# Kernel optimization log

Hardware: AMD Instinct MI355X
Metric: run time of the kernel (lower is better)

Reference implementation:

```python
import jax, jax.numpy as jnp
import numpy as np

N, E, F, H, L, G, C, NC = 100000, 1200000, 32, 64, 3, 256, 200000, 10
D = L * H  # concat node embedding dim = 192


def setup_inputs() -> dict:
    key = jax.random.key(0)
    ks = jax.random.split(key, 20)

    def w(k, shape):
        fan_in = shape[-2] if len(shape) > 1 else shape[0]
        return jax.random.normal(k, shape, jnp.float32) * (1.0 / np.sqrt(fan_in))

    inp = dict(
        x=jax.random.normal(ks[0], (N, F), jnp.float32),
        edge_index=jax.random.randint(ks[1], (2, E), 0, N),
        batch=jnp.sort(jax.random.randint(ks[2], (N,), 0, G)),
        cand_node=jax.random.randint(ks[3], (C,), 0, N),
        c1_W1=w(ks[4], (F, H)), c1_b1=jnp.zeros((H,)),
        c1_W2=w(ks[5], (H, H)), c1_b2=jnp.zeros((H,)),
        c1_g=jnp.ones((H,)), c1_be=jnp.zeros((H,)), c1_m=jnp.zeros((H,)), c1_v=jnp.ones((H,)),
        c1_eps=jnp.zeros((1,)),
        cs_W1=w(ks[6], (L - 1, H, H)), cs_b1=jnp.zeros((L - 1, H)),
        cs_W2=w(ks[7], (L - 1, H, H)), cs_b2=jnp.zeros((L - 1, H)),
        cs_g=jnp.ones((L - 1, H)), cs_be=jnp.zeros((L - 1, H)),
        cs_m=jnp.zeros((L - 1, H)), cs_v=jnp.ones((L - 1, H)),
        cs_eps=jnp.zeros((L - 1,)),
        nc_W1=w(ks[8], (D, 2 * H)), nc_b1=jnp.zeros((2 * H,)),
        nc_W2=w(ks[9], (2 * H, H)), nc_b2=jnp.zeros((H,)),
        nc_W3=w(ks[10], (H, H)), nc_b3=jnp.zeros((H,)),
        nc_W4=w(ks[11], (H, NC)), nc_b4=jnp.zeros((NC,)),
        comp_emb=jax.random.normal(ks[12], (NC, D), jnp.float32),
        ep_W1=w(ks[13], (2 * D, 2 * H)), ep_b1=jnp.zeros((2 * H,)),
        ep_W2=w(ks[14], (2 * H, H)), ep_b2=jnp.zeros((H,)),
        ep_W3=w(ks[15], (H, 1)), ep_b3=jnp.zeros((1,)),
    )
    return inp


def _bn(h, g, b, m, v):
    # BatchNorm1d in eval mode with running stats
    return g * (h - m) * jax.lax.rsqrt(v + 1e-5) + b


def _gin_layer(h, src, dst, eps, W1, b1, W2, b2, g, be, m, v):
    agg = jax.ops.segment_sum(h[src], dst, num_segments=N)  # sum aggregation
    h = (1.0 + eps) * h + agg
    h = jax.nn.relu(h @ W1 + b1)
    h = jax.nn.relu(h @ W2 + b2)
    return _bn(h, g, be, m, v)


def reference(x, edge_index, batch, cand_node,
              c1_W1, c1_b1, c1_W2, c1_b2, c1_g, c1_be, c1_m, c1_v, c1_eps,
              cs_W1, cs_b1, cs_W2, cs_b2, cs_g, cs_be, cs_m, cs_v, cs_eps,
              nc_W1, nc_b1, nc_W2, nc_b2, nc_W3, nc_b3, nc_W4, nc_b4,
              comp_emb, ep_W1, ep_b1, ep_W2, ep_b2, ep_W3, ep_b3):
    src, dst = edge_index[0], edge_index[1]
    # shared GIN encoder: concat per-layer node embeddings -> [N, L*H]
    h = _gin_layer(x, src, dst, c1_eps, c1_W1, c1_b1, c1_W2, c1_b2, c1_g, c1_be, c1_m, c1_v)
    xs = [h]
    for i in range(cs_W1.shape[0]):
        h = _gin_layer(h, src, dst, cs_eps[i], cs_W1[i], cs_b1[i], cs_W2[i], cs_b2[i],
                       cs_g[i], cs_be[i], cs_m[i], cs_v[i])
        xs.append(h)
    node_emb = jnp.concatenate(xs, axis=-1)  # [N, D]

    # global mean pool per graph -> classification head (dropout=identity in eval)
    sums = jax.ops.segment_sum(node_emb, batch, num_segments=G)
    cnt = jax.ops.segment_sum(jnp.ones((node_emb.shape[0], 1), node_emb.dtype), batch, num_segments=G)
    graph_emb = sums / jnp.maximum(cnt, 1.0)  # [G, D]
    hc = jax.nn.relu(graph_emb @ nc_W1 + nc_b1)
    hc = jax.nn.relu(hc @ nc_W2 + nc_b2)
    hc = jax.nn.relu(hc @ nc_W3 + nc_b3)
    logits = hc @ nc_W4 + nc_b4
    class_output = jax.nn.log_softmax(logits, axis=-1)  # [G, NC]

    # link prediction: predicted comp type per graph, score all candidates in one batch
    comp_idx = jnp.argmax(class_output, axis=-1)          # [G]
    cand_graph = batch[cand_node]                          # [C]
    ce = comp_emb[comp_idx[cand_graph]]                    # [C, D]
    de = node_emb[cand_node]                               # [C, D]
    ef = jnp.concatenate([ce, de], axis=-1)                # [C, 2D]
    he = jax.nn.relu(ef @ ep_W1 + ep_b1)
    he = jax.nn.relu(he @ ep_W2 + ep_b2)
    edge_scores = jax.nn.sigmoid((he @ ep_W3 + ep_b3).squeeze(-1))  # [C]
    return class_output, edge_scores
```

## Files before the change

kernel.cpp:

```cpp
#include <hip/hip_runtime.h>
#include <hip/hip_bf16.h>


#define GG 256
#define NCC 10
#define DD 192
#define BSH 8

typedef short bf16x8 __attribute__((ext_vector_type(8)));
typedef float f32x4  __attribute__((ext_vector_type(4)));

__device__ inline unsigned short f2bf_u(float x) {
    __hip_bfloat16 h = __float2bfloat16(x);
    return *reinterpret_cast<unsigned short*>(&h);
}
__device__ inline float bf2f(unsigned short u) {
    return __uint_as_float(((unsigned int)u) << 16);
}

__global__ void bin_hist(const int* __restrict__ dst, int* __restrict__ bcnt, int E_) {
    __shared__ int h[512];
    const int t = threadIdx.x;
    h[t] = 0; h[t + 256] = 0;
    __syncthreads();
    for (int e = blockIdx.x * 256 + t; e < E_; e += gridDim.x * 256)
        atomicAdd(&h[dst[e] >> BSH], 1);
    __syncthreads();
    if (h[t]) atomicAdd(&bcnt[t], h[t]);
    if (h[t + 256]) atomicAdd(&bcnt[t + 256], h[t + 256]);
}

__global__ void bin_scan(const int* __restrict__ bcnt, int* __restrict__ bbase,
                         int* __restrict__ bpos, int NB, int E_) {
    __shared__ int ps[256];
    const int t = threadIdx.x;
    int v0 = (2 * t < NB) ? bcnt[2 * t] : 0;
    int v1 = (2 * t + 1 < NB) ? bcnt[2 * t + 1] : 0;
    int pv = v0 + v1;
    ps[t] = pv;
    __syncthreads();
    for (int off = 1; off < 256; off <<= 1) {
        int x = (t >= off) ? ps[t - off] : 0;
        __syncthreads();
        ps[t] += x;
        __syncthreads();
    }
    const int excl = ps[t] - pv;
    if (2 * t < NB)     { bbase[2 * t] = excl;          bpos[2 * t] = excl; }
    if (2 * t + 1 < NB) { bbase[2 * t + 1] = excl + v0; bpos[2 * t + 1] = excl + v0; }
    if (t == 0) bbase[NB] = E_;
}

__global__ __launch_bounds__(256) void bin_scatter(
    const int* __restrict__ src, const int* __restrict__ dst,
    int* __restrict__ bpos, unsigned* __restrict__ ebuf, int E_) {
    __shared__ int h[512];
    __shared__ int base[512];
    const int t = threadIdx.x;
    const int e0 = blockIdx.x * 4096;
    h[t] = 0; h[t + 256] = 0;
    __syncthreads();
    int myb[16], myr[16];
    unsigned pk[16];
    #pragma unroll
    for (int u = 0; u < 16; ++u) {
        int e = e0 + t + u * 256;
        if (e < E_) {
            int d = dst[e];
            myb[u] = d >> BSH;
            pk[u] = ((unsigned)src[e] << BSH) | (unsigned)(d & ((1 << BSH) - 1));
            myr[u] = atomicAdd(&h[myb[u]], 1);
        } else myb[u] = -1;
    }
    __syncthreads();
    if (h[t]) base[t] = atomicAdd(&bpos[t], h[t]);
    if (h[t + 256]) base[t + 256] = atomicAdd(&bpos[t + 256], h[t + 256]);
    __syncthreads();
    #pragma unroll
    for (int u = 0; u < 16; ++u)
        if (myb[u] >= 0)
            ebuf[base[myb[u]] + myr[u]] = pk[u];
}

__global__ __launch_bounds__(256) void csr_bucket(
    const unsigned* __restrict__ ebuf, const int* __restrict__ bbase,
    int* __restrict__ rowptr, int* __restrict__ nbr, int N_, int NB) {
    __shared__ int lh[256];
    __shared__ int lx[256];
    __shared__ int ps[256];
    const int b = blockIdx.x;
    const int t = threadIdx.x;
    const int ebase = bbase[b], eend = bbase[b + 1];
    const int ecnt = eend - ebase;
    const int n0 = b << BSH;

    lh[t] = 0;
    __syncthreads();
    for (int i = t; i < ecnt; i += 256)
        atomicAdd(&lh[ebuf[ebase + i] & ((1 << BSH) - 1)], 1);
    __syncthreads();

    int v = lh[t];
    ps[t] = v;
    __syncthreads();
    for (int off = 1; off < 256; off <<= 1) {
        int x = (t >= off) ? ps[t - off] : 0;
        __syncthreads();
        ps[t] += x;
        __syncthreads();
    }
    lx[t] = ps[t] - v;
    {
        int n = n0 + t;
        if (n < N_) rowptr[n] = ebase + lx[t];
    }
    if (b == NB - 1 && t == 0) rowptr[N_] = eend;
    __syncthreads();
    lh[t] = lx[t];
    __syncthreads();
    for (int i = t; i < ecnt; i += 256) {
        unsigned p = ebuf[ebase + i];
        int r = atomicAdd(&lh[p & ((1 << BSH) - 1)], 1);
        nbr[ebase + r] = (int)(p >> BSH);
    }
}

__global__ void x2b_kernel(const float* __restrict__ x, unsigned short* __restrict__ xb,
                           int n_elem) {
    int i = blockIdx.x * 256 + threadIdx.x;
    int stride = gridDim.x * 256;
    for (; i * 4 < n_elem; i += stride) {
        float4 v = *(const float4*)(x + i * 4);
        ushort4 u;
        u.x = f2bf_u(v.x); u.y = f2bf_u(v.y); u.z = f2bf_u(v.z); u.w = f2bf_u(v.w);
        *(ushort4*)(xb + i * 4) = u;
    }
}

__global__ void prep_enc(const float* __restrict__ c1W1, const float* __restrict__ c1W2,
                         const float* __restrict__ csW1, const float* __restrict__ csW2,
                         unsigned short* __restrict__ enc) {
    int idx = blockIdx.x * 256 + threadIdx.x;
    if (idx >= 22528) return;
    const float* W; int rel;
    if (idx < 2048)       { W = c1W1;        rel = idx; }
    else if (idx < 6144)  { W = c1W2;        rel = idx - 2048; }
    else if (idx < 10240) { W = csW1;        rel = idx - 6144; }
    else if (idx < 14336) { W = csW2;        rel = idx - 10240; }
    else if (idx < 18432) { W = csW1 + 4096; rel = idx - 14336; }
    else                  { W = csW2 + 4096; rel = idx - 18432; }
    int frag = rel >> 9;
    int lane = (rel >> 3) & 63;
    int j = rel & 7;
    int ks = frag >> 2, nt = frag & 3;
    int k = ks * 32 + ((lane >> 4) << 3) + j;
    int n = nt * 16 + (lane & 15);
    enc[idx] = f2bf_u(W[k * 64 + n]);
}

__global__ void gcnt_bs(const int* __restrict__ batch, int* __restrict__ gcnt_i, int N_) {
    __shared__ int lbs[GG + 1];
    const int g = threadIdx.x;
    int lo = 0, hi = N_;
    while (lo < hi) {
        int mid = (lo + hi) >> 1;
        if (batch[mid] < g) lo = mid + 1; else hi = mid;
    }
    lbs[g] = lo;
    if (g == 0) lbs[GG] = N_;
    __syncthreads();
    gcnt_i[g] = lbs[g + 1] - lbs[g];
}

#define SWZ(row, byte) ((byte) ^ (((row) & 7) << 4))

#define GSTEP(VCUR, VNXT)                                                     \
    _Pragma("unroll")                                                         \
    for (int u = 0; u < 16; ++u)                                              \
        VNXT[u] = bf2f(*(const unsigned short*)(hbase + (unsigned)idx[u] * (unsigned)RSB + lane2)); \
    _Pragma("unroll")                                                         \
    for (int u = 0; u < 16; ++u) idx[u] = nbp[k + 32 + u];                    \
    {                                                                         \
        float runk = run;                                                     \
        _Pragma("unroll")                                                     \
        for (int u = 0; u < 16; ++u) run += VCUR[u];                          \
        if ((unsigned)(e1 - k) < 16u) { float tt = runk;                      \
            _Pragma("unroll")                                                 \
            for (int u = 0; u < 16; ++u) tt += (u < e1 - k) ? VCUR[u] : 0.f;  \
            s0 = tt; }                                                        \
        if ((unsigned)(e2 - k) < 16u) { float tt = runk;                      \
            _Pragma("unroll")                                                 \
            for (int u = 0; u < 16; ++u) tt += (u < e2 - k) ? VCUR[u] : 0.f;  \
            s1 = tt; }                                                        \
        if ((unsigned)(e3 - k) < 16u) { float tt = runk;                      \
            _Pragma("unroll")                                                 \
            for (int u = 0; u < 16; ++u) tt += (u < e3 - k) ? VCUR[u] : 0.f;  \
            s2 = tt; }                                                        \
        if ((unsigned)(cnt - k) < 16u) { float tt = runk;                     \
            _Pragma("unroll")                                                 \
            for (int u = 0; u < 16; ++u) tt += (u < cnt - k) ? VCUR[u] : 0.f; \
            s3 = tt; }                                                        \
    }                                                                         \
    k += 16;                                                                  \
    if (k > cnt) break;

template<int K>
__global__ __launch_bounds__(512) void gin_fused(
    const unsigned short* __restrict__ hin_b,
    const int* __restrict__ rowptr, const int* __restrict__ nbr,
    const unsigned short* __restrict__ W1p, const float* __restrict__ b1,
    const unsigned short* __restrict__ W2p, const float* __restrict__ b2,
    const float* __restrict__ gamma, const float* __restrict__ beta,
    const float* __restrict__ mean, const float* __restrict__ var,
    const float* __restrict__ eps_p,
    __hip_bfloat16* __restrict__ out_b,
    const int* __restrict__ batch, float* __restrict__ gsum, int soff,
    int N_) {
    __shared__ char s_agg[32 * 128];
    __shared__ char s_h1[32 * 128];
    __shared__ char s_out[32 * 128];
    __shared__ int sb[32];

    const int t = threadIdx.x;
    const int lane = t & 63;
    const int w = t >> 6;
    const int node0 = blockIdx.x * 32;
    const int nb = w * 4;

    if (t < 32) sb[t] = (node0 + t < N_) ? batch[node0 + t] : -1;

    const float eps1 = 1.0f + eps_p[0];

    const int n0w = node0 + nb;
    const int rp0 = __builtin_amdgcn_readfirstlane(rowptr[min(n0w + 0, N_)]);
    const int rp1 = __builtin_amdgcn_readfirstlane(rowptr[min(n0w + 1, N_)]);
    const int rp2 = __builtin_amdgcn_readfirstlane(rowptr[min(n0w + 2, N_)]);
    const int rp3 = __builtin_amdgcn_readfirstlane(rowptr[min(n0w + 3, N_)]);
    const int rp4 = __builtin_amdgcn_readfirstlane(rowptr[min(n0w + 4, N_)]);
    const int cnt = rp4 - rp0;
    const int e1 = rp1 - rp0, e2 = rp2 - rp0, e3 = rp3 - rp0;
    const int* nbp = nbr + rp0;

    const int RSB = (K == 64) ? DD * 2 : 64;
    const int OST = (K == 64) ? DD : 32;
    const char* hbase = (const char*)hin_b;
    const unsigned lane2 = (unsigned)(lane & (K - 1)) * 2u;

    int idx[16];
    float vA[16], vB[16];
    float run = 0.f, s0 = 0.f, s1 = 0.f, s2 = 0.f, s3 = 0.f;
    #pragma unroll
    for (int u = 0; u < 16; ++u) idx[u] = nbp[u];
    #pragma unroll
    for (int u = 0; u < 16; ++u)
        vA[u] = bf2f(*(const unsigned short*)(hbase + (unsigned)idx[u] * (unsigned)RSB + lane2));
    #pragma unroll
    for (int u = 0; u < 16; ++u) idx[u] = nbp[16 + u];
    for (int k = 0;;) {
        GSTEP(vA, vB)
        GSTEP(vB, vA)
    }
    float a0 = s0, a1 = s1 - s0, a2 = s2 - s1, a3 = s3 - s2;
    {
        const unsigned short* hbp = hin_b + (lane & (K - 1));
        if (n0w + 0 < N_) a0 += eps1 * bf2f(hbp[(size_t)(n0w + 0) * OST]);
        if (n0w + 1 < N_) a1 += eps1 * bf2f(hbp[(size_t)(n0w + 1) * OST]);
        if (n0w + 2 < N_) a2 += eps1 * bf2f(hbp[(size_t)(n0w + 2) * OST]);
        if (n0w + 3 < N_) a3 += eps1 * bf2f(hbp[(size_t)(n0w + 3) * OST]);
    }
    if (K == 64 || lane < 32) {
        const int kd = lane & (K - 1);
        *(unsigned short*)(s_agg + SWZ(nb + 0, (nb + 0) * 128 + kd * 2)) = f2bf_u(a0);
        *(unsigned short*)(s_agg + SWZ(nb + 1, (nb + 1) * 128 + kd * 2)) = f2bf_u(a1);
        *(unsigned short*)(s_agg + SWZ(nb + 2, (nb + 2) * 128 + kd * 2)) = f2bf_u(a2);
        *(unsigned short*)(s_agg + SWZ(nb + 3, (nb + 3) * 128 + kd * 2)) = f2bf_u(a3);
    }
    __syncthreads();

    const int mt = w >> 2, nt = w & 3;
    const int arow = mt * 16 + (lane & 15);
    const int col = nt * 16 + (lane & 15);
    f32x4 c1v = (f32x4){0.f, 0.f, 0.f, 0.f};
    #pragma unroll
    for (int ks = 0; ks < K / 32; ++ks) {
        bf16x8 a = *(const bf16x8*)(s_agg + SWZ(arow, arow * 128 + ks * 64 + ((lane >> 4) << 4)));
        bf16x8 b = *(const bf16x8*)(W1p + (((ks << 2) + nt) << 9) + (lane << 3));
        c1v = __builtin_amdgcn_mfma_f32_16x16x32_bf16(a, b, c1v, 0, 0, 0);
    }
    {
        const float bb1 = b1[col];
        #pragma unroll
        for (int reg = 0; reg < 4; ++reg) {
            int row = mt * 16 + ((lane >> 4) << 2) + reg;
            float v = fmaxf(c1v[reg] + bb1, 0.f);
            *(unsigned short*)(s_h1 + SWZ(row, row * 128 + col * 2)) = f2bf_u(v);
        }
    }
    __syncthreads();

    f32x4 c2v = (f32x4){0.f, 0.f, 0.f, 0.f};
    #pragma unroll
    for (int ks = 0; ks < 2; ++ks) {
        bf16x8 a = *(const bf16x8*)(s_h1 + SWZ(arow, arow * 128 + ks * 64 + ((lane >> 4) << 4)));
        bf16x8 b = *(const bf16x8*)(W2p + (((ks << 2) + nt) << 9) + (lane << 3));
        c2v = __builtin_amdgcn_mfma_f32_16x16x32_bf16(a, b, c2v, 0, 0, 0);
    }
    {
        const float bb2 = b2[col];
        const float ga = gamma[col], bet = beta[col], mu = mean[col];
        const float iv = rsqrtf(var[col] + 1e-5f);
        #pragma unroll
        for (int reg = 0; reg < 4; ++reg) {
            int row = mt * 16 + ((lane >> 4) << 2) + reg;
            float v = fmaxf(c2v[reg] + bb2, 0.f);
            v = ga * (v - mu) * iv + bet;
            *(unsigned short*)(s_out + SWZ(row, row * 128 + col * 2)) = f2bf_u(v);
        }
    }
    __syncthreads();

    {
        int r = t >> 4, c8 = t & 15;
        int node = node0 + r;
        if (node < N_) {
            ushort4 v = *(const ushort4*)(s_out + SWZ(r, r * 128 + c8 * 8));
            *(ushort4*)((unsigned short*)out_b + (size_t)node * DD + c8 * 4) = v;
        }
    }

    if (t < 256) {
        const int d = t & 63;
        const int rg = t >> 6;
        float acc = 0.f;
        int curg = sb[rg * 8];
        #pragma unroll
        for (int r = rg * 8; r < rg * 8 + 8; ++r) {
            int g = sb[r];
            if (g != curg) {
                if (curg >= 0) atomicAdd(&gsum[curg * DD + soff + d], acc);
                acc = 0.f; curg = g;
            }
            if (g >= 0)
                acc += bf2f(*(const unsigned short*)(s_out + SWZ(r, r * 128 + d * 2)));
        }
        if (curg >= 0) atomicAdd(&gsum[curg * DD + soff + d], acc);
    }
}

__global__ void head_kernel(const float* __restrict__ gsum, const int* __restrict__ gcnt_i,
                            const float* __restrict__ W1, const float* __restrict__ b1,
                            const float* __restrict__ W2, const float* __restrict__ b2,
                            const float* __restrict__ W3, const float* __restrict__ b3,
                            const float* __restrict__ W4, const float* __restrict__ b4,
                            float* __restrict__ class_out, int* __restrict__ comp_idx) {
    const int g = blockIdx.x;
    const int t = threadIdx.x;
    __shared__ float ge[DD], h1[128], h2[64], h3[64], logits[NCC];

    const float c = fmaxf((float)gcnt_i[g], 1.0f);
    if (t < DD) ge[t] = gsum[g * DD + t] / c;
    __syncthreads();

    if (t < 128) {
        float a = b1[t];
        #pragma unroll 4
        for (int k = 0; k < DD; ++k) a += ge[k] * W1[k * 128 + t];
        h1[t] = fmaxf(a, 0.0f);
    }
    __syncthreads();
    if (t < 64) {
        float a = b2[t];
        #pragma unroll 4
        for (int k = 0; k < 128; ++k) a += h1[k] * W2[k * 64 + t];
        h2[t] = fmaxf(a, 0.0f);
    }
    __syncthreads();
    if (t < 64) {
        float a = b3[t];
        #pragma unroll 4
        for (int k = 0; k < 64; ++k) a += h2[k] * W3[k * 64 + t];
        h3[t] = fmaxf(a, 0.0f);
    }
    __syncthreads();
    if (t < NCC) {
        float a = b4[t];
        #pragma unroll
        for (int k = 0; k < 64; ++k) a += h3[k] * W4[k * NCC + t];
        logits[t] = a;
    }
    __syncthreads();
    if (t == 0) {
        float mx = logits[0]; int am = 0;
        for (int j = 1; j < NCC; ++j) if (logits[j] > mx) { mx = logits[j]; am = j; }
        float se = 0.0f;
        for (int j = 0; j < NCC; ++j) se += expf(logits[j] - mx);
        float lse = logf(se);
        for (int j = 0; j < NCC; ++j) class_out[g * NCC + j] = logits[j] - mx - lse;
        comp_idx[g] = am;
    }
}

__global__ void prep_edge(const float* __restrict__ W1, const float* __restrict__ b1,
                          const float* __restrict__ W2, const float* __restrict__ comp_emb,
                          unsigned short* __restrict__ W1b_p, unsigned short* __restrict__ W2_p,
                          float* __restrict__ pc) {
    int idx = blockIdx.x * 256 + threadIdx.x;
    const int S1 = 6 * 8 * 512;
    const int S2 = 4 * 4 * 512;
    if (idx < S1) {
        int frag = idx >> 9;
        int lane = (idx >> 3) & 63;
        int j = idx & 7;
        int kstep = frag >> 3, nt = frag & 7;
        int k = kstep * 32 + ((lane >> 4) << 3) + j;
        int n = nt * 16 + (lane & 15);
        W1b_p[idx] = f2bf_u(W1[(192 + k) * 128 + n]);
    } else if (idx < S1 + S2) {
        int i2 = idx - S1;
        int frag = i2 >> 9;
        int lane = (i2 >> 3) & 63;
        int j = i2 & 7;
        int kstep = frag >> 2, nt = frag & 3;
        int k = kstep * 32 + ((lane >> 4) << 3) + j;
        int n = nt * 16 + (lane & 15);
        W2_p[i2] = f2bf_u(W2[k * 64 + n]);
    } else if (idx < S1 + S2 + NCC * 128) {
        int i3 = idx - (S1 + S2);
        int ci = i3 >> 7, col = i3 & 127;
        float a = b1[col];
        for (int k = 0; k < DD; ++k) a += comp_emb[ci * DD + k] * W1[k * 128 + col];
        pc[i3] = a;
    }
}

__global__ __launch_bounds__(256, 5) void edge_mfma(
    const int* __restrict__ cand, const int* __restrict__ batch,
    const int* __restrict__ comp_idx, const short* __restrict__ hb,
    const unsigned short* __restrict__ W1b_p, const unsigned short* __restrict__ W2_p,
    const float* __restrict__ pc, const float* __restrict__ W3,
    const float* __restrict__ b3, float* __restrict__ scores, int C_) {
    __shared__ char s_buf[64 * 384];
    __shared__ float s_part[4][64];
    __shared__ int s_node[64];
    __shared__ int s_ci[64];
    __shared__ float s_w3[64];

    const int t = threadIdx.x;
    const int lane = t & 63;
    const int w = t >> 6;
    const int c0 = blockIdx.x * 64;

    if (t < 64) {
        int c = c0 + t;
        int node = (c < C_) ? cand[c] : cand[0];
        s_node[t] = node;
        s_ci[t] = comp_idx[batch[node]];
        s_w3[t] = W3[t];
    }
    __syncthreads();

    for (int i = t; i < 64 * 24; i += 256) {
        int r = i / 24, c8 = i - r * 24;
        bf16x8 v = *(const bf16x8*)(hb + (size_t)s_node[r] * DD + c8 * 8);
        *(bf16x8*)(s_buf + SWZ(r, r * 384 + c8 * 16)) = v;
    }
    __syncthreads();

    f32x4 acc1[4][2];
    #pragma unroll
    for (int rt = 0; rt < 4; ++rt)
        #pragma unroll
        for (int b = 0; b < 2; ++b) acc1[rt][b] = (f32x4){0.f, 0.f, 0.f, 0.f};
    #pragma unroll
    for (int ks = 0; ks < 6; ++ks) {
        bf16x8 b0 = *(const bf16x8*)(W1b_p + ((ks * 8 + 2 * w + 0) << 9) + (lane << 3));
        bf16x8 b1f = *(const bf16x8*)(W1b_p + ((ks * 8 + 2 * w + 1) << 9) + (lane << 3));
        #pragma unroll
        for (int rt = 0; rt < 4; ++rt) {
            int arow = rt * 16 + (lane & 15);
            bf16x8 a = *(const bf16x8*)(s_buf + SWZ(arow, arow * 384 + ks * 64 + ((lane >> 4) << 4)));
            acc1[rt][0] = __builtin_amdgcn_mfma_f32_16x16x32_bf16(a, b0, acc1[rt][0], 0, 0, 0);
            acc1[rt][1] = __builtin_amdgcn_mfma_f32_16x16x32_bf16(a, b1f, acc1[rt][1], 0, 0, 0);
        }
    }
    __syncthreads();

    #pragma unroll
    for (int rt = 0; rt < 4; ++rt) {
        #pragma unroll
        for (int reg = 0; reg < 4; ++reg) {
            int row = rt * 16 + ((lane >> 4) << 2) + reg;
            int ci = s_ci[row];
            #pragma unroll
            for (int b = 0; b < 2; ++b) {
                int col = (2 * w + b) * 16 + (lane & 15);
                float v = fmaxf(acc1[rt][b][reg] + pc[ci * 128 + col], 0.f);
                *(unsigned short*)(s_buf + SWZ(row, row * 256 + col * 2)) = f2bf_u(v);
            }
        }
    }
    __syncthreads();

    f32x4 acc2[4];
    #pragma unroll
    for (int rt = 0; rt < 4; ++rt) acc2[rt] = (f32x4){0.f, 0.f, 0.f, 0.f};
    #pragma unroll
    for (int ks = 0; ks < 4; ++ks) {
        bf16x8 b = *(const bf16x8*)(W2_p + ((ks * 4 + w) << 9) + (lane << 3));
        #pragma unroll
        for (int rt = 0; rt < 4; ++rt) {
            int arow = rt * 16 + (lane & 15);
            bf16x8 a = *(const bf16x8*)(s_buf + SWZ(arow, arow * 256 + ks * 64 + ((lane >> 4) << 4)));
            acc2[rt] = __builtin_amdgcn_mfma_f32_16x16x32_bf16(a, b, acc2[rt], 0, 0, 0);
        }
    }

    {
        const float w3v = s_w3[w * 16 + (lane & 15)];
        #pragma unroll
        for (int rt = 0; rt < 4; ++rt) {
            #pragma unroll
            for (int reg = 0; reg < 4; ++reg) {
                float p = fmaxf(acc2[rt][reg], 0.f) * w3v;
                p += __shfl_xor(p, 1);
                p += __shfl_xor(p, 2);
                p += __shfl_xor(p, 4);
                p += __shfl_xor(p, 8);
                if ((lane & 15) == 0)
                    s_part[w][rt * 16 + ((lane >> 4) << 2) + reg] = p;
            }
        }
    }
    __syncthreads();

    if (t < 64) {
        int c = c0 + t;
        if (c < C_) {
            float p = s_part[0][t] + s_part[1][t] + s_part[2][t] + s_part[3][t] + b3[0];
            scores[c] = 1.0f / (1.0f + expf(-p));
        }
    }
}

extern "C" void kernel_launch(void* const* d_in, const int* in_sizes, int n_in,
                              void* d_out, int out_size, void* d_ws, size_t ws_size,
                              hipStream_t stream) {
    const float* x        = (const float*)d_in[0];
    const int*   ei       = (const int*)d_in[1];
    const int*   batch    = (const int*)d_in[2];
    const int*   cand     = (const int*)d_in[3];
    const float* c1_W1    = (const float*)d_in[4];
    const float* c1_b1    = (const float*)d_in[5];
    const float* c1_W2    = (const float*)d_in[6];
    const float* c1_b2    = (const float*)d_in[7];
    const float* c1_g     = (const float*)d_in[8];
    const float* c1_be    = (const float*)d_in[9];
    const float* c1_m     = (const float*)d_in[10];
    const float* c1_v     = (const float*)d_in[11];
    const float* c1_eps   = (const float*)d_in[12];
    const float* cs_W1    = (const float*)d_in[13];
    const float* cs_b1    = (const float*)d_in[14];
    const float* cs_W2    = (const float*)d_in[15];
    const float* cs_b2    = (const float*)d_in[16];
    const float* cs_g     = (const float*)d_in[17];
    const float* cs_be    = (const float*)d_in[18];
    const float* cs_m     = (const float*)d_in[19];
    const float* cs_v     = (const float*)d_in[20];
    const float* cs_eps   = (const float*)d_in[21];
    const float* nc_W1    = (const float*)d_in[22];
    const float* nc_b1    = (const float*)d_in[23];
    const float* nc_W2    = (const float*)d_in[24];
    const float* nc_b2    = (const float*)d_in[25];
    const float* nc_W3    = (const float*)d_in[26];
    const float* nc_b3    = (const float*)d_in[27];
    const float* nc_W4    = (const float*)d_in[28];
    const float* nc_b4    = (const float*)d_in[29];
    const float* comp_emb = (const float*)d_in[30];
    const float* ep_W1    = (const float*)d_in[31];
    const float* ep_b1    = (const float*)d_in[32];
    const float* ep_W2    = (const float*)d_in[33];
    const float* ep_b2    = (const float*)d_in[34];
    const float* ep_W3    = (const float*)d_in[35];
    const float* ep_b3    = (const float*)d_in[36];

    const int N_ = in_sizes[0] / 32;
    const int E_ = in_sizes[1] / 2;
    const int C_ = in_sizes[3];
    const int* src = ei;
    const int* dst = ei + E_;
    const int NB = (N_ + (1 << BSH) - 1) >> BSH;

    char* ws = (char*)d_ws;
    size_t off = 0;
    __hip_bfloat16* hb = (__hip_bfloat16*)(ws + off); off += (size_t)N_ * DD * 2;
    unsigned short* xb = (unsigned short*)(ws + off); off += (size_t)N_ * 32 * 2;
    int*   rowptr   = (int*)(ws + off);   off += (size_t)(N_ + 2) * 4;
    int*   nbr      = (int*)(ws + off);   off += (size_t)(E_ + 128) * 4;
    int*   bcnt     = (int*)(ws + off);   off += 2048;
    int*   bbase    = (int*)(ws + off);   off += 2080;
    int*   bpos     = (int*)(ws + off);   off += 2048;
    float* gsum     = (float*)(ws + off); off += (size_t)GG * DD * 4;
    int*   gcnt_i   = (int*)(ws + off);   off += 1024;
    int*   comp_idx = (int*)(ws + off);   off += 1024;
    float* pc       = (float*)(ws + off); off += NCC * 128 * 4;
    unsigned short* W1b_p = (unsigned short*)(ws + off); off += 6 * 8 * 512 * 2;
    unsigned short* W2_p  = (unsigned short*)(ws + off); off += 4 * 4 * 512 * 2;
    unsigned short* enc   = (unsigned short*)(ws + off); off += 22528 * 2;
    unsigned* ebuf  = (unsigned*)hb;

    float* class_out = (float*)d_out;
    float* scores    = class_out + GG * NCC;

    prep_edge<<<(6 * 8 * 512 + 4 * 4 * 512 + NCC * 128 + 255) / 256, 256, 0, stream>>>(
        ep_W1, ep_b1, ep_W2, comp_emb, W1b_p, W2_p, pc);
    prep_enc<<<(22528 + 255) / 256, 256, 0, stream>>>(c1_W1, c1_W2, cs_W1, cs_W2, enc);
    x2b_kernel<<<2048, 256, 0, stream>>>(x, xb, N_ * 32);

    hipMemsetAsync(bcnt, 0, 2048, stream);
    hipMemsetAsync(nbr + E_, 0, 128 * 4, stream);
    bin_hist<<<1024, 256, 0, stream>>>(dst, bcnt, E_);
    bin_scan<<<1, 256, 0, stream>>>(bcnt, bbase, bpos, NB, E_);
    bin_scatter<<<(E_ + 4095) / 4096, 256, 0, stream>>>(src, dst, bpos, ebuf, E_);
    csr_bucket<<<NB, 256, 0, stream>>>(ebuf, bbase, rowptr, nbr, N_, NB);

    hipMemsetAsync(gsum, 0, (size_t)GG * DD * 4, stream);
    gcnt_bs<<<1, GG, 0, stream>>>(batch, gcnt_i, N_);

    const int gblk = (N_ + 31) / 32;
    gin_fused<32><<<gblk, 512, 0, stream>>>(
        xb, rowptr, nbr,
        enc + 0, c1_b1, enc + 2048, c1_b2,
        c1_g, c1_be, c1_m, c1_v, c1_eps, hb + 0, batch, gsum, 0, N_);
    gin_fused<64><<<gblk, 512, 0, stream>>>(
        (const unsigned short*)hb + 0, rowptr, nbr,
        enc + 6144, cs_b1 + 0, enc + 10240, cs_b2 + 0,
        cs_g + 0, cs_be + 0, cs_m + 0, cs_v + 0, cs_eps + 0, hb + 64, batch, gsum, 64, N_);
    gin_fused<64><<<gblk, 512, 0, stream>>>(
        (const unsigned short*)hb + 64, rowptr, nbr,
        enc + 14336, cs_b1 + 64, enc + 18432, cs_b2 + 64,
        cs_g + 64, cs_be + 64, cs_m + 64, cs_v + 64, cs_eps + 1, hb + 128, batch, gsum, 128, N_);

    head_kernel<<<GG, 256, 0, stream>>>(gsum, gcnt_i, nc_W1, nc_b1, nc_W2, nc_b2,
                                        nc_W3, nc_b3, nc_W4, nc_b4, class_out, comp_idx);

    edge_mfma<<<(C_ + 63) / 64, 256, 0, stream>>>(
        cand, batch, comp_idx, (const short*)hb, W1b_p, W2_p, pc, ep_W3, ep_b3, scores, C_);
}
```

Baseline: 286.8 us.

## Merge prep kernels and memsets into fewer launches; widen CSR buckets

Folds the weight-packing, x-to-bf16 conversion and bcnt/nbr-pad zeroing into one prep_all launch. Folds the bin scan, per-graph count binary search and gsum zeroing into one scan_misc launch, which removes several kernel launches and memset calls. BSH goes from 8 to 9, so each csr_bucket block handles 512 nodes and there are half as many buckets; bin_hist also runs with fewer blocks. The risk is lower parallelism in the CSR build and more bucket index range relative to the 512-entry histograms.

```diff
diff --git a/kernel.cpp b/kernel.cpp
--- a/kernel.cpp
+++ b/kernel.cpp
@@ -5,7 +5,11 @@
 #define GG 256
 #define NCC 10
 #define DD 192
-#define BSH 8
+#define BSH 9
+
+#define PE_BLK 133
+#define EN_BLK 88
+#define XB_BLK 512
 
 typedef short bf16x8 __attribute__((ext_vector_type(8)));
 typedef float f32x4  __attribute__((ext_vector_type(4)));
@@ -16,6 +20,76 @@
 }
 __device__ inline float bf2f(unsigned short u) {
     return __uint_as_float(((unsigned int)u) << 16);
+}
+
+__global__ void prep_all(
+    const float* __restrict__ epW1, const float* __restrict__ epb1,
+    const float* __restrict__ epW2, const float* __restrict__ comp_emb,
+    unsigned short* __restrict__ W1b_p, unsigned short* __restrict__ W2_p,
+    float* __restrict__ pc,
+    const float* __restrict__ c1W1, const float* __restrict__ c1W2,
+    const float* __restrict__ csW1, const float* __restrict__ csW2,
+    unsigned short* __restrict__ enc,
+    const float* __restrict__ x, unsigned short* __restrict__ xb, int nx4,
+    int* __restrict__ bcnt, int* __restrict__ nbrpad) {
+    const int b = blockIdx.x, t = threadIdx.x;
+    if (b < PE_BLK) {
+        int idx = b * 256 + t;
+        const int S1 = 6 * 8 * 512;
+        const int S2 = 4 * 4 * 512;
+        if (idx < S1) {
+            int frag = idx >> 9;
+            int lane = (idx >> 3) & 63;
+            int j = idx & 7;
+            int kstep = frag >> 3, nt = frag & 7;
+            int k = kstep * 32 + ((lane >> 4) << 3) + j;
+            int n = nt * 16 + (lane & 15);
+            W1b_p[idx] = f2bf_u(epW1[(192 + k) * 128 + n]);
+        } else if (idx < S1 + S2) {
+            int i2 = idx - S1;
+            int frag = i2 >> 9;
+            int lane = (i2 >> 3) & 63;
+            int j = i2 & 7;
+            int kstep = frag >> 2, nt = frag & 3;
+            int k = kstep * 32 + ((lane >> 4) << 3) + j;
+            int n = nt * 16 + (lane & 15);
+            W2_p[i2] = f2bf_u(epW2[k * 64 + n]);
+        } else if (idx < S1 + S2 + NCC * 128) {
+            int i3 = idx - (S1 + S2);
+            int ci = i3 >> 7, col = i3 & 127;
+            float a = epb1[col];
+            for (int k = 0; k < DD; ++k) a += comp_emb[ci * DD + k] * epW1[k * 128 + col];
+            pc[i3] = a;
+        }
+    } else if (b < PE_BLK + EN_BLK) {
+        int idx = (b - PE_BLK) * 256 + t;
+        if (idx < 22528) {
+            const float* W; int rel;
+            if (idx < 2048)       { W = c1W1;        rel = idx; }
+            else if (idx < 6144)  { W = c1W2;        rel = idx - 2048; }
+            else if (idx < 10240) { W = csW1;        rel = idx - 6144; }
+            else if (idx < 14336) { W = csW2;        rel = idx - 10240; }
+            else if (idx < 18432) { W = csW1 + 4096; rel = idx - 14336; }
+            else                  { W = csW2 + 4096; rel = idx - 18432; }
+            int frag = rel >> 9;
+            int lane = (rel >> 3) & 63;
+            int j = rel & 7;
+            int ks = frag >> 2, nt = frag & 3;
+            int k = ks * 32 + ((lane >> 4) << 3) + j;
+            int n = nt * 16 + (lane & 15);
+            enc[idx] = f2bf_u(W[k * 64 + n]);
+        }
+    } else if (b < PE_BLK + EN_BLK + XB_BLK) {
+        for (int i = (b - PE_BLK - EN_BLK) * 256 + t; i < nx4; i += XB_BLK * 256) {
+            float4 v = *(const float4*)(x + i * 4);
+            ushort4 u;
+            u.x = f2bf_u(v.x); u.y = f2bf_u(v.y); u.z = f2bf_u(v.z); u.w = f2bf_u(v.w);
+            *(ushort4*)(xb + i * 4) = u;
+        }
+    } else {
+        bcnt[t] = 0; bcnt[t + 256] = 0;
+        if (t < 128) nbrpad[t] = 0;
+    }
 }
 
 __global__ void bin_hist(const int* __restrict__ dst, int* __restrict__ bcnt, int E_) {
@@ -30,25 +104,43 @@
     if (h[t + 256]) atomicAdd(&bcnt[t + 256], h[t + 256]);
 }
 
-__global__ void bin_scan(const int* __restrict__ bcnt, int* __restrict__ bbase,
-                         int* __restrict__ bpos, int NB, int E_) {
-    __shared__ int ps[256];
-    const int t = threadIdx.x;
-    int v0 = (2 * t < NB) ? bcnt[2 * t] : 0;
-    int v1 = (2 * t + 1 < NB) ? bcnt[2 * t + 1] : 0;
-    int pv = v0 + v1;
-    ps[t] = pv;
-    __syncthreads();
-    for (int off = 1; off < 256; off <<= 1) {
-        int x = (t >= off) ? ps[t - off] : 0;
+__global__ void scan_misc(const int* __restrict__ bcnt, int* __restrict__ bbase,
+                          int* __restrict__ bpos, int NB, int E_,
+                          const int* __restrict__ batch, int* __restrict__ gcnt_i,
+                          float* __restrict__ gsum, int N_) {
+    const int b = blockIdx.x, t = threadIdx.x;
+    if (b == 0) {
+        __shared__ int ps[256];
+        int v0 = (2 * t < NB) ? bcnt[2 * t] : 0;
+        int v1 = (2 * t + 1 < NB) ? bcnt[2 * t + 1] : 0;
+        int pv = v0 + v1;
+        ps[t] = pv;
         __syncthreads();
-        ps[t] += x;
+        for (int off = 1; off < 256; off <<= 1) {
+            int x = (t >= off) ? ps[t - off] : 0;
+            __syncthreads();
+            ps[t] += x;
+            __syncthreads();
+        }
+        const int excl = ps[t] - pv;
+        if (2 * t < NB)     { bbase[2 * t] = excl;          bpos[2 * t] = excl; }
+        if (2 * t + 1 < NB) { bbase[2 * t + 1] = excl + v0; bpos[2 * t + 1] = excl + v0; }
+        if (t == 0) bbase[NB] = E_;
+    } else if (b == 1) {
+        __shared__ int lbs[GG + 1];
+        int lo = 0, hi = N_;
+        while (lo < hi) {
+            int mid = (lo + hi) >> 1;
+            if (batch[mid] < t) lo = mid + 1; else hi = mid;
+        }
+        lbs[t] = lo;
+        if (t == 0) lbs[GG] = N_;
         __syncthreads();
-    }
-    const int excl = ps[t] - pv;
-    if (2 * t < NB)     { bbase[2 * t] = excl;          bpos[2 * t] = excl; }
-    if (2 * t + 1 < NB) { bbase[2 * t + 1] = excl + v0; bpos[2 * t + 1] = excl + v0; }
-    if (t == 0) bbase[NB] = E_;
+        gcnt_i[t] = lbs[t + 1] - lbs[t];
+    } else {
+        int i = (b - 2) * 256 + t;
+        if (i < GG * DD) gsum[i] = 0.f;
+    }
 }
 
 __global__ __launch_bounds__(256) void bin_scatter(
@@ -85,23 +177,24 @@
 __global__ __launch_bounds__(256) void csr_bucket(
     const unsigned* __restrict__ ebuf, const int* __restrict__ bbase,
     int* __restrict__ rowptr, int* __restrict__ nbr, int N_, int NB) {
-    __shared__ int lh[256];
-    __shared__ int lx[256];
+    __shared__ int lh[512];
+    __shared__ int lx[512];
     __shared__ int ps[256];
     const int b = blockIdx.x;
     const int t = threadIdx.x;
     const int ebase = bbase[b], eend = bbase[b + 1];
     const int ecnt = eend - ebase;
     const int n0 = b << BSH;
-
-    lh[t] = 0;
+    const unsigned M = (1 << BSH) - 1;
+
+    for (int i = t; i < 512; i += 256) lh[i] = 0;
     __syncthreads();
     for (int i = t; i < ecnt; i += 256)
-        atomicAdd(&lh[ebuf[ebase + i] & ((1 << BSH) - 1)], 1);
-    __syncthreads();
-
-    int v = lh[t];
-    ps[t] = v;
+        atomicAdd(&lh[ebuf[ebase + i] & M], 1);
+    __syncthreads();
+
+    int pv = lh[2 * t] + lh[2 * t + 1];
+    ps[t] = pv;
     __syncthreads();
     for (int off = 1; off < 256; off <<= 1) {
         int x = (t >= off) ? ps[t - off] : 0;
@@ -109,67 +202,24 @@
         ps[t] += x;
         __syncthreads();
     }
-    lx[t] = ps[t] - v;
-    {
-        int n = n0 + t;
-        if (n < N_) rowptr[n] = ebase + lx[t];
+    const int excl = ps[t] - pv;
+    lx[2 * t] = excl;
+    lx[2 * t + 1] = excl + lh[2 * t];
+    __syncthreads();
+
+    for (int i = t; i < 512; i += 256) {
+        int n = n0 + i;
+        if (n < N_) rowptr[n] = ebase + lx[i];
     }
     if (b == NB - 1 && t == 0) rowptr[N_] = eend;
     __syncthreads();
-    lh[t] = lx[t];
+    for (int i = t; i < 512; i += 256) lh[i] = lx[i];
     __syncthreads();
     for (int i = t; i < ecnt; i += 256) {
         unsigned p = ebuf[ebase + i];
-        int r = atomicAdd(&lh[p & ((1 << BSH) - 1)], 1);
+        int r = atomicAdd(&lh[p & M], 1);
         nbr[ebase + r] = (int)(p >> BSH);
     }
-}
-
-__global__ void x2b_kernel(const float* __restrict__ x, unsigned short* __restrict__ xb,
-                           int n_elem) {
-    int i = blockIdx.x * 256 + threadIdx.x;
-    int stride = gridDim.x * 256;
-    for (; i * 4 < n_elem; i += stride) {
-        float4 v = *(const float4*)(x + i * 4);
-        ushort4 u;
-        u.x = f2bf_u(v.x); u.y = f2bf_u(v.y); u.z = f2bf_u(v.z); u.w = f2bf_u(v.w);
-        *(ushort4*)(xb + i * 4) = u;
-    }
-}
-
-__global__ void prep_enc(const float* __restrict__ c1W1, const float* __restrict__ c1W2,
-                         const float* __restrict__ csW1, const float* __restrict__ csW2,
-                         unsigned short* __restrict__ enc) {
-    int idx = blockIdx.x * 256 + threadIdx.x;
-    if (idx >= 22528) return;
-    const float* W; int rel;
-    if (idx < 2048)       { W = c1W1;        rel = idx; }
-    else if (idx < 6144)  { W = c1W2;        rel = idx - 2048; }
-    else if (idx < 10240) { W = csW1;        rel = idx - 6144; }
-    else if (idx < 14336) { W = csW2;        rel = idx - 10240; }
-    else if (idx < 18432) { W = csW1 + 4096; rel = idx - 14336; }
-    else                  { W = csW2 + 4096; rel = idx - 18432; }
-    int frag = rel >> 9;
-    int lane = (rel >> 3) & 63;
-    int j = rel & 7;
-    int ks = frag >> 2, nt = frag & 3;
-    int k = ks * 32 + ((lane >> 4) << 3) + j;
-    int n = nt * 16 + (lane & 15);
-    enc[idx] = f2bf_u(W[k * 64 + n]);
-}
-
-__global__ void gcnt_bs(const int* __restrict__ batch, int* __restrict__ gcnt_i, int N_) {
-    __shared__ int lbs[GG + 1];
-    const int g = threadIdx.x;
-    int lo = 0, hi = N_;
-    while (lo < hi) {
-        int mid = (lo + hi) >> 1;
-        if (batch[mid] < g) lo = mid + 1; else hi = mid;
-    }
-    lbs[g] = lo;
-    if (g == 0) lbs[GG] = N_;
-    __syncthreads();
-    gcnt_i[g] = lbs[g + 1] - lbs[g];
 }
 
 #define SWZ(row, byte) ((byte) ^ (((row) & 7) << 4))
@@ -397,39 +447,6 @@
         float lse = logf(se);
         for (int j = 0; j < NCC; ++j) class_out[g * NCC + j] = logits[j] - mx - lse;
         comp_idx[g] = am;
-    }
-}
-
-__global__ void prep_edge(const float* __restrict__ W1, const float* __restrict__ b1,
-                          const float* __restrict__ W2, const float* __restrict__ comp_emb,
-                          unsigned short* __restrict__ W1b_p, unsigned short* __restrict__ W2_p,
-                          float* __restrict__ pc) {
-    int idx = blockIdx.x * 256 + threadIdx.x;
-    const int S1 = 6 * 8 * 512;
-    const int S2 = 4 * 4 * 512;
-    if (idx < S1) {
-        int frag = idx >> 9;
-        int lane = (idx >> 3) & 63;
-        int j = idx & 7;
-        int kstep = frag >> 3, nt = frag & 7;
-        int k = kstep * 32 + ((lane >> 4) << 3) + j;
-        int n = nt * 16 + (lane & 15);
-        W1b_p[idx] = f2bf_u(W1[(192 + k) * 128 + n]);
-    } else if (idx < S1 + S2) {
-        int i2 = idx - S1;
-        int frag = i2 >> 9;
-        int lane = (i2 >> 3) & 63;
-        int j = i2 & 7;
-        int kstep = frag >> 2, nt = frag & 3;
-        int k = kstep * 32 + ((lane >> 4) << 3) + j;
-        int n = nt * 16 + (lane & 15);
-        W2_p[i2] = f2bf_u(W2[k * 64 + n]);
-    } else if (idx < S1 + S2 + NCC * 128) {
-        int i3 = idx - (S1 + S2);
-        int ci = i3 >> 7, col = i3 & 127;
-        float a = b1[col];
-        for (int k = 0; k < DD; ++k) a += comp_emb[ci * DD + k] * W1[k * 128 + col];
-        pc[i3] = a;
     }
 }
 
@@ -611,20 +628,16 @@
     float* class_out = (float*)d_out;
     float* scores    = class_out + GG * NCC;
 
-    prep_edge<<<(6 * 8 * 512 + 4 * 4 * 512 + NCC * 128 + 255) / 256, 256, 0, stream>>>(
-        ep_W1, ep_b1, ep_W2, comp_emb, W1b_p, W2_p, pc);
-    prep_enc<<<(22528 + 255) / 256, 256, 0, stream>>>(c1_W1, c1_W2, cs_W1, cs_W2, enc);
-    x2b_kernel<<<2048, 256, 0, stream>>>(x, xb, N_ * 32);
-
-    hipMemsetAsync(bcnt, 0, 2048, stream);
-    hipMemsetAsync(nbr + E_, 0, 128 * 4, stream);
-    bin_hist<<<1024, 256, 0, stream>>>(dst, bcnt, E_);
-    bin_scan<<<1, 256, 0, stream>>>(bcnt, bbase, bpos, NB, E_);
+    prep_all<<<PE_BLK + EN_BLK + XB_BLK + 1, 256, 0, stream>>>(
+        ep_W1, ep_b1, ep_W2, comp_emb, W1b_p, W2_p, pc,
+        c1_W1, c1_W2, cs_W1, cs_W2, enc,
+        x, xb, N_ * 32 / 4, bcnt, nbr + E_);
+
+    bin_hist<<<256, 256, 0, stream>>>(dst, bcnt, E_);
+    scan_misc<<<2 + (GG * DD + 255) / 256, 256, 0, stream>>>(
+        bcnt, bbase, bpos, NB, E_, batch, gcnt_i, gsum, N_);
     bin_scatter<<<(E_ + 4095) / 4096, 256, 0, stream>>>(src, dst, bpos, ebuf, E_);
     csr_bucket<<<NB, 256, 0, stream>>>(ebuf, bbase, rowptr, nbr, N_, NB);
-
-    hipMemsetAsync(gsum, 0, (size_t)GG * DD * 4, stream);
-    gcnt_bs<<<1, GG, 0, stream>>>(batch, gcnt_i, N_);
 
     const int gblk = (N_ + 31) / 32;
     gin_fused<32><<<gblk, 512, 0, stream>>>(
```

Result: faster. 249.2 us (-13.1%).
